# Performance work log

Hardware: AMD Instinct MI355X
Metric: run time of the kernel (lower is better)

## Reference

```python
import jax, jax.numpy as jnp
import numpy as np

B, T, N, S = 32, 64, 2048, 2048
DEMB = DENC = DDEC = 256


def setup_inputs() -> dict:
    key = jax.random.key(0)
    ks = jax.random.split(key, 14)
    u = lambda k, shp, s=0.05: jax.random.uniform(k, shp, jnp.float32, -s, s)
    return {
        "emb": jax.random.normal(ks[0], (B, N, DEMB), jnp.float32),
        "emb_mask": jnp.ones((B, N), jnp.float32),
        "enc": jax.random.normal(ks[1], (B, S, DENC), jnp.float32),
        "enc_mask": jnp.ones((B, S), jnp.float32),
        "gt": jax.random.randint(ks[2], (B, T), 0, N),
        "go": jax.random.uniform(ks[3], (DEMB,), jnp.float32, -0.1, 0.1),
        "Wih": u(ks[4], (4 * DDEC, DEMB)),
        "Whh": u(ks[5], (4 * DDEC, DDEC)),
        "bih": u(ks[6], (4 * DDEC,)),
        "bhh": u(ks[7], (4 * DDEC,)),
        "Wdt": u(ks[8], (DENC, DDEC)),
        "bdt": u(ks[9], (DENC,)),
        "Wf": u(ks[10], (DEMB + 1, DENC + DDEC)),
        "bf": u(ks[11], (DEMB + 1,)),
    }


def _pointer_decode(emb, emb_mask, enc, enc_mask, gt, go, Wih, Whh, bih, bhh, Wdt, bdt, Wf, bf):
    b, n, demb = emb.shape
    t = gt.shape[1]
    h = Whh.shape[1]
    # picked_t at step t is the (clipped) one-hot sum of gt[:, :t] (exclusive)
    onehot = jax.nn.one_hot(gt, n, dtype=emb.dtype)              # [B,T,N]
    picked = jnp.clip(jnp.cumsum(onehot, axis=1) - onehot, 0.0, 1.0)
    # teacher-forced LSTM inputs: go at t=0, then emb gathered at gt[:, t-1]
    prev = jnp.take_along_axis(emb, gt[:, :-1, None], axis=1)    # [B,T-1,demb]
    x = jnp.concatenate([jnp.broadcast_to(go, (b, 1, demb)), prev], axis=1)

    def cell(carry, x_t):
        h_t, c_t = carry
        g = x_t @ Wih.T + bih + h_t @ Whh.T + bhh                # [B,4H]
        i, f, gg, o = jnp.split(g, 4, axis=-1)                   # torch gate order i,f,g,o
        c_new = jax.nn.sigmoid(f) * c_t + jax.nn.sigmoid(i) * jnp.tanh(gg)
        h_new = jax.nn.sigmoid(o) * jnp.tanh(c_new)
        return (h_new, c_new), h_new

    h0 = jnp.zeros((b, h), emb.dtype)
    _, hs = jax.lax.scan(cell, (h0, h0), jnp.swapaxes(x, 0, 1))
    hs = jnp.swapaxes(hs, 0, 1)                                  # [B,T,H]
    # DotAttn: project dec state to denc, masked softmax over enc positions
    dec = hs @ Wdt.T + bdt                                       # [B,T,denc]
    raw = jnp.einsum('btd,bsd->bts', dec, enc)
    raw = raw - (1.0 - enc_mask)[:, None, :] * 1e20
    w = jax.nn.softmax(raw, axis=-1)
    attn = jnp.einsum('bts,bsd->btd', w, enc)                    # [B,T,denc]
    feat = jnp.concatenate([hs, attn], axis=-1) @ Wf.T + bf      # [B,T,demb+1]
    # pointer score: feat . concat([emb, picked]) over last dim, split to avoid [B,T,N,demb+1]
    score = jnp.einsum('btk,bnk->btn', feat[..., :demb], emb)
    score = score + feat[..., -1][:, :, None] * picked
    score = score - (1.0 - emb_mask)[:, None, :] * 1e20
    return score                                                 # [B,T,N]


def reference(emb, emb_mask, enc, enc_mask, gt, go, Wih, Whh, bih, bhh, Wdt, bdt, Wf, bf):
    return _pointer_decode(emb, emb_mask, enc, enc_mask, gt, go, Wih, Whh, bih, bhh, Wdt, bdt, Wf, bf)
```

## Files before the change

kernel.cpp:

```cpp
#include <hip/hip_runtime.h>
#include <cstddef>

#define BB 32
#define TT 64
#define NN_ 2048
#define SS 2048
#define DD 256
#define GG 1024
#define LP 32
#define FLD 264

typedef __attribute__((ext_vector_type(8))) short short8;
typedef __attribute__((ext_vector_type(4))) float f32x4;

static __device__ inline unsigned short f2bf(float f) {
    union { float f; unsigned int u; } v; v.f = f;
    unsigned int u = v.u;
    unsigned int r = u + 0x7FFF + ((u >> 16) & 1);
    return (unsigned short)(r >> 16);
}

static __device__ inline short8 pack8(float4 a, float4 b) {
    short8 s;
    s[0] = (short)f2bf(a.x); s[1] = (short)f2bf(a.y);
    s[2] = (short)f2bf(a.z); s[3] = (short)f2bf(a.w);
    s[4] = (short)f2bf(b.x); s[5] = (short)f2bf(b.y);
    s[6] = (short)f2bf(b.z); s[7] = (short)f2bf(b.w);
    return s;
}

static __device__ inline bool ok32(unsigned int v) {
    unsigned int x = v ^ 0x7F807F80u;
    return (((x - 0x00010001u) & ~x & 0x80008000u) == 0u);
}


__global__ __launch_bounds__(256) void k_gather(const float* __restrict__ emb,
                                                const int* __restrict__ gt,
                                                const float* __restrict__ go,
                                                float* __restrict__ x) {
    int idx = blockIdx.x * 256 + threadIdx.x;
    int d = idx & (DD - 1);
    int t = (idx >> 8) & (TT - 1);
    int b = idx >> 14;
    float v;
    if (t == 0) v = go[d];
    else        v = emb[((size_t)b * NN_ + gt[b * TT + t - 1]) * DD + d];
    x[idx] = v;
}

__global__ __launch_bounds__(256) void k_first_init(int* __restrict__ firstpos) {
    int idx = blockIdx.x * 256 + threadIdx.x;
    firstpos[idx] = TT;
}

__global__ __launch_bounds__(256) void k_first_min(const int* __restrict__ gt,
                                                   int* __restrict__ firstpos) {
    int idx = blockIdx.x * 256 + threadIdx.x;
    int b = idx / TT;
    int t = idx % TT;
    atomicMin(&firstpos[(size_t)b * NN_ + gt[idx]], t);
}

__global__ __launch_bounds__(256) void k_poison(unsigned int* __restrict__ hbuf32) {
    hbuf32[blockIdx.x * 256 + threadIdx.x] = 0x7F807F80u;
}

__global__ __launch_bounds__(256) void k_h2f(const unsigned int* __restrict__ hbuf32,
                                             float* __restrict__ hs) {
    int idx = blockIdx.x * 256 + threadIdx.x;
    int j = idx & 255;
    int t = (idx >> 8) & 63;
    int b = idx >> 14;
    unsigned int w = hbuf32[(size_t)t * 4096 + (j >> 1) * 32 + b];
    unsigned short h = (j & 1) ? (unsigned short)(w >> 16) : (unsigned short)(w & 0xFFFF);
    union { unsigned int u; float f; } v;
    v.u = ((unsigned int)h) << 16;
    hs[idx] = v.f;
}

__global__ __launch_bounds__(256) void k_cat(const float* __restrict__ hs,
                                             const float* __restrict__ attn,
                                             float* __restrict__ cat) {
    int idx = blockIdx.x * 256 + threadIdx.x;
    int d = idx & 511;
    int bt = idx >> 9;
    cat[idx] = (d < DD) ? hs[(size_t)bt * DD + d]
                        : attn[(size_t)bt * DD + (d - DD)];
}

__global__ __launch_bounds__(256) void gemm_bf16_nt(
        const float* __restrict__ A, const float* __restrict__ Bm,
        float* __restrict__ C, int K, int lda, int ldb, int ldc,
        long sA, long sB, long sC, int Nlim,
        const float* __restrict__ bias1, const float* __restrict__ bias2,
        const int* __restrict__ firstpos, const float* __restrict__ emb_mask,
        int fscol) {
    int bz = blockIdx.z;
    A += (size_t)bz * sA; Bm += (size_t)bz * sB; C += (size_t)bz * sC;
    int tm = blockIdx.y * 64, tn = blockIdx.x * 64;
    __shared__ short Ab[64][72];
    __shared__ short Bb[64][72];
    __shared__ float sfs[64];
    int tid = threadIdx.x, lane = tid & 63, wid = tid >> 6;
    int wm = wid & 1, wn = wid >> 1;

    if (fscol >= 0 && tid < 64) sfs[tid] = A[(size_t)(tm + tid) * lda + fscol];

    f32x4 zero = {0.f, 0.f, 0.f, 0.f};
    f32x4 acc[2][2] = {{zero, zero}, {zero, zero}};

    int row = tid >> 2, kk = (tid & 3) * 16;
    int brow = tn + row; if (brow >= Nlim) brow = Nlim - 1;
    const float* ap = &A[(size_t)(tm + row) * lda + kk];
    const float* bp = &Bm[(size_t)brow * ldb + kk];

    for (int k0 = 0; k0 < K; k0 += 64) {
        float4 a0 = *(const float4*)(ap + k0);
        float4 a1 = *(const float4*)(ap + k0 + 4);
        float4 a2 = *(const float4*)(ap + k0 + 8);
        float4 a3 = *(const float4*)(ap + k0 + 12);
        float4 b0 = *(const float4*)(bp + k0);
        float4 b1 = *(const float4*)(bp + k0 + 4);
        float4 b2 = *(const float4*)(bp + k0 + 8);
        float4 b3 = *(const float4*)(bp + k0 + 12);
        *(short8*)&Ab[row][kk]     = pack8(a0, a1);
        *(short8*)&Ab[row][kk + 8] = pack8(a2, a3);
        *(short8*)&Bb[row][kk]     = pack8(b0, b1);
        *(short8*)&Bb[row][kk + 8] = pack8(b2, b3);
        __syncthreads();
#pragma unroll
        for (int kt = 0; kt < 2; ++kt) {
            int k8 = kt * 32 + (lane >> 4) * 8;
            short8 fa0 = *(const short8*)&Ab[wm * 32 + (lane & 15)][k8];
            short8 fa1 = *(const short8*)&Ab[wm * 32 + 16 + (lane & 15)][k8];
            short8 fb0 = *(const short8*)&Bb[wn * 32 + (lane & 15)][k8];
            short8 fb1 = *(const short8*)&Bb[wn * 32 + 16 + (lane & 15)][k8];
            acc[0][0] = __builtin_amdgcn_mfma_f32_16x16x32_bf16(fa0, fb0, acc[0][0], 0, 0, 0);
            acc[0][1] = __builtin_amdgcn_mfma_f32_16x16x32_bf16(fa0, fb1, acc[0][1], 0, 0, 0);
            acc[1][0] = __builtin_amdgcn_mfma_f32_16x16x32_bf16(fa1, fb0, acc[1][0], 0, 0, 0);
            acc[1][1] = __builtin_amdgcn_mfma_f32_16x16x32_bf16(fa1, fb1, acc[1][1], 0, 0, 0);
        }
        __syncthreads();
    }

#pragma unroll
    for (int i = 0; i < 2; ++i) {
#pragma unroll
        for (int j = 0; j < 2; ++j) {
#pragma unroll
            for (int r = 0; r < 4; ++r) {
                int lrow = wm * 32 + i * 16 + (lane >> 4) * 4 + r;
                int gcol = tn + wn * 32 + j * 16 + (lane & 15);
                if (gcol < Nlim) {
                    float v = acc[i][j][r];
                    if (bias1) v += bias1[gcol];
                    if (bias2) v += bias2[gcol];
                    if (firstpos) {
                        int grow = tm + lrow;
                        if (firstpos[(size_t)bz * NN_ + gcol] < grow) v += sfs[lrow];
                        v -= (1.0f - emb_mask[(size_t)bz * NN_ + gcol]) * 1e20f;
                    }
                    C[(size_t)(tm + lrow) * ldc + gcol] = v;
                }
            }
        }
    }
}

__global__ __launch_bounds__(256) void gemm_attn(const float* __restrict__ W,
                                                 const float* __restrict__ enc,
                                                 float* __restrict__ attn) {
    int b = blockIdx.z;
    int tn = blockIdx.x * 64;
    const float* Wb = W + (size_t)b * TT * SS;
    const float* Eb = enc + (size_t)b * SS * DD;
    float* Cb = attn + (size_t)b * TT * DD;
    __shared__ short As[64][72];
    __shared__ float Bs[64][66];
    int tid = threadIdx.x, lane = tid & 63, wid = tid >> 6;
    int wm = wid & 1, wn = wid >> 1;
    f32x4 zero = {0.f, 0.f, 0.f, 0.f};
    f32x4 acc[2][2] = {{zero, zero}, {zero, zero}};
    int row = tid >> 2, kk = (tid & 3) * 16;
    const float* ap = Wb + (size_t)row * SS + kk;
    const float* bp = Eb + (size_t)row * DD + tn + kk;

    for (int k0 = 0; k0 < SS; k0 += 64) {
        float4 a0 = *(const float4*)(ap + k0);
        float4 a1 = *(const float4*)(ap + k0 + 4);
        float4 a2 = *(const float4*)(ap + k0 + 8);
        float4 a3 = *(const float4*)(ap + k0 + 12);
        *(short8*)&As[row][kk]     = pack8(a0, a1);
        *(short8*)&As[row][kk + 8] = pack8(a2, a3);
        const float* bq = bp + (size_t)k0 * DD;
#pragma unroll
        for (int i = 0; i < 8; ++i)
            *(float2*)&Bs[row][kk + 2 * i] = *(const float2*)(bq + 2 * i);
        __syncthreads();
#pragma unroll
        for (int kt = 0; kt < 2; ++kt) {
            int k8 = kt * 32 + (lane >> 4) * 8;
            short8 fa0 = *(const short8*)&As[wm * 32 + (lane & 15)][k8];
            short8 fa1 = *(const short8*)&As[wm * 32 + 16 + (lane & 15)][k8];
            short8 fb0, fb1;
#pragma unroll
            for (int e = 0; e < 8; ++e) {
                fb0[e] = (short)f2bf(Bs[k8 + e][wn * 32 + (lane & 15)]);
                fb1[e] = (short)f2bf(Bs[k8 + e][wn * 32 + 16 + (lane & 15)]);
            }
            acc[0][0] = __builtin_amdgcn_mfma_f32_16x16x32_bf16(fa0, fb0, acc[0][0], 0, 0, 0);
            acc[0][1] = __builtin_amdgcn_mfma_f32_16x16x32_bf16(fa0, fb1, acc[0][1], 0, 0, 0);
            acc[1][0] = __builtin_amdgcn_mfma_f32_16x16x32_bf16(fa1, fb0, acc[1][0], 0, 0, 0);
            acc[1][1] = __builtin_amdgcn_mfma_f32_16x16x32_bf16(fa1, fb1, acc[1][1], 0, 0, 0);
        }
        __syncthreads();
    }

#pragma unroll
    for (int i = 0; i < 2; ++i)
#pragma unroll
        for (int j = 0; j < 2; ++j)
#pragma unroll
            for (int r = 0; r < 4; ++r) {
                int lrow = wm * 32 + i * 16 + (lane >> 4) * 4 + r;
                int gcol = tn + wn * 32 + j * 16 + (lane & 15);
                Cb[(size_t)lrow * DD + gcol] = acc[i][j][r];
            }
}

__global__ __launch_bounds__(256) void k_lstm_mfma(const float* __restrict__ xW,
                                                   const float* __restrict__ Whh,
                                                   unsigned int* __restrict__ hbuf32) {
    int p = blockIdx.x;
    int tid = threadIdx.x;
    int lane = tid & 63;
    int wid = tid >> 6;
    int mi = wid & 1;
    int ni = wid >> 1;
    int jj = lane >> 4;
    int bl = lane & 15;
    int j = p * 8 + mi * 4 + jj;
    int b = ni * 16 + bl;

    short8 afrag[8];
    {
        int rr = lane & 15;
        const float* wrow = Whh + (size_t)((rr & 3) * 256 + p * 8 + mi * 4 + (rr >> 2)) * DD;
#pragma unroll
        for (int kt = 0; kt < 8; ++kt) {
            short8 f;
#pragma unroll
            for (int e = 0; e < 8; ++e)
                f[e] = (short)f2bf(wrow[kt * 32 + (lane >> 4) * 8 + e]);
            afrag[kt] = f;
        }
    }

    float cstate = 0.0f;
    const int wb = jj * 128 + b;

    for (int t = 0; t < TT; ++t) {
        const float* g0 = xW + ((size_t)b * TT + t) * GG + j;
        float xb0 = g0[0], xb1 = g0[256], xb2 = g0[512], xb3 = g0[768];

        f32x4 acc = {0.f, 0.f, 0.f, 0.f};
        if (t > 0) {
            const unsigned int* hb = hbuf32 + (size_t)(t - 1) * 4096;
            unsigned int q[32];
            bool ready = false;
            while (!ready) {
                ready = true;
#pragma unroll
                for (int kt = 0; kt < 8; ++kt)
#pragma unroll
                    for (int w4 = 0; w4 < 4; ++w4)
                        q[kt * 4 + w4] = __hip_atomic_load(&hb[kt * 512 + wb + w4 * 32],
                            __ATOMIC_RELAXED, __HIP_MEMORY_SCOPE_AGENT);
#pragma unroll
                for (int i = 0; i < 32; ++i) ready = ready && ok32(q[i]);
            }
#pragma unroll
            for (int kt = 0; kt < 8; ++kt) {
                union { unsigned int w[4]; short8 s; } u;
                u.w[0] = q[kt * 4 + 0]; u.w[1] = q[kt * 4 + 1];
                u.w[2] = q[kt * 4 + 2]; u.w[3] = q[kt * 4 + 3];
                acc = __builtin_amdgcn_mfma_f32_16x16x32_bf16(afrag[kt], u.s, acc, 0, 0, 0);
            }
        }

        float pi = xb0 + acc[0];
        float pf = xb1 + acc[1];
        float pg = xb2 + acc[2];
        float po = xb3 + acc[3];
        float ig = 1.0f / (1.0f + __expf(-pi));
        float fg = 1.0f / (1.0f + __expf(-pf));
        float gg = tanhf(pg);
        float og = 1.0f / (1.0f + __expf(-po));
        cstate = fg * cstate + ig * gg;
        float hn = og * tanhf(cstate);

        float hnb = __shfl_down(hn, 16);
        if ((jj & 1) == 0) {
            unsigned int wv = (unsigned int)f2bf(hn) |
                              ((unsigned int)f2bf(hnb) << 16);
            __hip_atomic_store(&hbuf32[(size_t)t * 4096 +
                                       (p * 4 + mi * 2 + (jj >> 1)) * 32 + b],
                               wv, __ATOMIC_RELAXED, __HIP_MEMORY_SCOPE_AGENT);
        }
        asm volatile("s_waitcnt vmcnt(0)" ::: "memory");
    }
}

__global__ __launch_bounds__(256) void k_softmax(float* __restrict__ raw,
                                                 const float* __restrict__ enc_mask) {
    int bt = blockIdx.x;
    int b = bt / TT;
    float* r = raw + (size_t)bt * SS;
    __shared__ float row[SS];
    __shared__ float red[16];
    int tid = threadIdx.x;
    float mx = -1e30f;
    for (int s = tid; s < SS; s += 256) {
        float v = r[s] - (1.0f - enc_mask[(size_t)b * SS + s]) * 1e20f;
        row[s] = v;
        mx = fmaxf(mx, v);
    }
#pragma unroll
    for (int o = 32; o > 0; o >>= 1) mx = fmaxf(mx, __shfl_down(mx, o));
    if ((tid & 63) == 0) red[tid >> 6] = mx;
    __syncthreads();
    if (tid == 0) {
        float m2 = red[0];
        for (int i = 1; i < 4; ++i) m2 = fmaxf(m2, red[i]);
        red[0] = m2;
    }
    __syncthreads();
    mx = red[0];
    float sum = 0.0f;
    for (int s = tid; s < SS; s += 256) {
        float e = expf(row[s] - mx);
        row[s] = e;
        sum += e;
    }
#pragma unroll
    for (int o = 32; o > 0; o >>= 1) sum += __shfl_down(sum, o);
    if ((tid & 63) == 0) red[8 + (tid >> 6)] = sum;
    __syncthreads();
    if (tid == 0) {
        float s = red[8];
        for (int i = 1; i < 4; ++i) s += red[8 + i];
        red[8] = s;
    }
    __syncthreads();
    float inv = 1.0f / red[8];
    for (int s = tid; s < SS; s += 256) r[s] = row[s] * inv;
}

extern "C" void kernel_launch(void* const* d_in, const int* in_sizes, int n_in,
                              void* d_out, int out_size, void* d_ws, size_t ws_size,
                              hipStream_t stream) {
    const float* emb      = (const float*)d_in[0];
    const float* emb_mask = (const float*)d_in[1];
    const float* enc      = (const float*)d_in[2];
    const float* enc_mask = (const float*)d_in[3];
    const int*   gt       = (const int*)d_in[4];
    const float* go       = (const float*)d_in[5];
    const float* Wih      = (const float*)d_in[6];
    const float* Whh      = (const float*)d_in[7];
    const float* bih      = (const float*)d_in[8];
    const float* bhh      = (const float*)d_in[9];
    const float* Wdt      = (const float*)d_in[10];
    const float* bdt      = (const float*)d_in[11];
    const float* Wf       = (const float*)d_in[12];
    const float* bf       = (const float*)d_in[13];
    float* out = (float*)d_out;

    float* ws    = (float*)d_ws;
    float* x     = ws;
    float* xW    = x     + (size_t)BB * TT * DD;
    float* hs    = xW    + (size_t)BB * TT * GG;
    float* dec   = hs    + (size_t)BB * TT * DD;
    float* w     = dec   + (size_t)BB * TT * DD;
    float* attn  = w     + (size_t)BB * TT * SS;
    float* feat  = attn  + (size_t)BB * TT * DD;
    float* cat   = feat  + (size_t)BB * TT * FLD;
    float* cat_end = cat + (size_t)BB * TT * 512;
    int* firstpos = (int*)cat_end;
    unsigned int* hbuf32 = (unsigned int*)(firstpos + (size_t)BB * NN_);

    k_gather<<<BB * TT * DD / 256, 256, 0, stream>>>(emb, gt, go, x);
    k_first_init<<<BB * NN_ / 256, 256, 0, stream>>>(firstpos);
    k_first_min<<<BB * TT / 256, 256, 0, stream>>>(gt, firstpos);
    k_poison<<<TT * 128 * 32 / 256, 256, 0, stream>>>(hbuf32);

    gemm_bf16_nt<<<dim3(GG / 64, BB * TT / 64, 1), 256, 0, stream>>>(
        x, Wih, xW, DD, DD, DD, GG, 0, 0, 0, GG,
        bih, bhh, nullptr, nullptr, -1);

    k_lstm_mfma<<<LP, 256, 0, stream>>>(xW, Whh, hbuf32);

    k_h2f<<<BB * TT * DD / 256, 256, 0, stream>>>(hbuf32, hs);

    gemm_bf16_nt<<<dim3(DD / 64, BB * TT / 64, 1), 256, 0, stream>>>(
        hs, Wdt, dec, DD, DD, DD, DD, 0, 0, 0, DD,
        bdt, nullptr, nullptr, nullptr, -1);

    gemm_bf16_nt<<<dim3(SS / 64, 1, BB), 256, 0, stream>>>(
        dec, enc, w, DD, DD, DD, SS,
        (long)TT * DD, (long)SS * DD, (long)TT * SS, SS,
        nullptr, nullptr, nullptr, nullptr, -1);

    k_softmax<<<BB * TT, 256, 0, stream>>>(w, enc_mask);

    gemm_attn<<<dim3(DD / 64, 1, BB), 256, 0, stream>>>(w, enc, attn);

    k_cat<<<BB * TT * 512 / 256, 256, 0, stream>>>(hs, attn, cat);

    gemm_bf16_nt<<<dim3(5, BB * TT / 64, 1), 256, 0, stream>>>(
        cat, Wf, feat, 2 * DD, 2 * DD, 2 * DD, FLD, 0, 0, 0, DD + 1,
        bf, nullptr, nullptr, nullptr, -1);

    gemm_bf16_nt<<<dim3(NN_ / 64, 1, BB), 256, 0, stream>>>(
        feat, emb, out, DD, FLD, DD, NN_,
        (long)TT * FLD, (long)NN_ * DD, (long)TT * NN_, NN_,
        nullptr, nullptr, firstpos, emb_mask, 256);
}
```

Baseline: 308.6 us.

## Replace cross-block LSTM with per-batch block using fp16 dot2 and shared memory

Replaces the 32-block MFMA LSTM, which spun on poisoned global-memory flags to exchange the hidden state across blocks every timestep, with one 1024-thread block per batch row that keeps Whh (fp16-packed, 128 registers per thread) local. The hidden state is exchanged through LDS with __syncthreads, and the gate preactivations are computed with fdot2. This removes the grid-wide polling, the poison and h2f kernels, and global atomics, and writes fp32 hs directly. The cost is heavy register pressure (128 weight registers at 1024 threads), scalar dot products instead of MFMA, fp16 rounding of weights and hidden state, and a new Whh transpose kernel.

Result: slower. 378.8 us (+22.8%).

```diff
diff --git a/kernel.cpp b/kernel.cpp
--- a/kernel.cpp
+++ b/kernel.cpp
@@ -7,11 +7,11 @@
 #define SS 2048
 #define DD 256
 #define GG 1024
-#define LP 32
 #define FLD 264
 
 typedef __attribute__((ext_vector_type(8))) short short8;
 typedef __attribute__((ext_vector_type(4))) float f32x4;
+typedef _Float16 h2_t __attribute__((ext_vector_type(2)));
 
 static __device__ inline unsigned short f2bf(float f) {
     union { float f; unsigned int u; } v; v.f = f;
@@ -29,9 +29,29 @@
     return s;
 }
 
-static __device__ inline bool ok32(unsigned int v) {
-    unsigned int x = v ^ 0x7F807F80u;
-    return (((x - 0x00010001u) & ~x & 0x80008000u) == 0u);
+static __device__ inline h2_t as_h2(unsigned int u) {
+    union { unsigned int u; h2_t h; } v; v.u = u; return v.h;
+}
+static __device__ inline unsigned int h2_pack(float a, float b) {
+    union { unsigned int u; h2_t h; } v;
+    v.h[0] = (_Float16)a; v.h[1] = (_Float16)b; return v.u;
+}
+
+#if __has_builtin(__builtin_amdgcn_fdot2)
+static __device__ inline float fdot2(h2_t a, h2_t b, float c) {
+    return __builtin_amdgcn_fdot2(a, b, c, false);
+}
+#else
+static __device__ inline float fdot2(h2_t a, h2_t b, float c) {
+    return c + (float)a[0] * (float)b[0] + (float)a[1] * (float)b[1];
+}
+#endif
+
+static __device__ inline float sigm(float x) { return 1.0f / (1.0f + __expf(-x)); }
+static __device__ inline float tanh_f(float x) {
+    float xc = fminf(fmaxf(x, -20.0f), 20.0f);
+    float e = __expf(-2.0f * xc);
+    return (1.0f - e) / (1.0f + e);
 }
 
 
@@ -62,21 +82,13 @@
     atomicMin(&firstpos[(size_t)b * NN_ + gt[idx]], t);
 }
 
-__global__ __launch_bounds__(256) void k_poison(unsigned int* __restrict__ hbuf32) {
-    hbuf32[blockIdx.x * 256 + threadIdx.x] = 0x7F807F80u;
-}
-
-__global__ __launch_bounds__(256) void k_h2f(const unsigned int* __restrict__ hbuf32,
-                                             float* __restrict__ hs) {
+__global__ __launch_bounds__(256) void k_whhT16(const float* __restrict__ Whh,
+                                                unsigned int* __restrict__ WhhT16) {
     int idx = blockIdx.x * 256 + threadIdx.x;
-    int j = idx & 255;
-    int t = (idx >> 8) & 63;
-    int b = idx >> 14;
-    unsigned int w = hbuf32[(size_t)t * 4096 + (j >> 1) * 32 + b];
-    unsigned short h = (j & 1) ? (unsigned short)(w >> 16) : (unsigned short)(w & 0xFFFF);
-    union { unsigned int u; float f; } v;
-    v.u = ((unsigned int)h) << 16;
-    hs[idx] = v.f;
+    int k2 = idx & 127;
+    int g = idx >> 7;
+    float2 w = *(const float2*)(Whh + (size_t)g * DD + 2 * k2);
+    WhhT16[(size_t)k2 * GG + g] = h2_pack(w.x, w.y);
 }
 
 __global__ __launch_bounds__(256) void k_cat(const float* __restrict__ hs,
@@ -229,86 +241,53 @@
             }
 }
 
-__global__ __launch_bounds__(256) void k_lstm_mfma(const float* __restrict__ xW,
-                                                   const float* __restrict__ Whh,
-                                                   unsigned int* __restrict__ hbuf32) {
-    int p = blockIdx.x;
-    int tid = threadIdx.x;
-    int lane = tid & 63;
-    int wid = tid >> 6;
-    int mi = wid & 1;
-    int ni = wid >> 1;
-    int jj = lane >> 4;
-    int bl = lane & 15;
-    int j = p * 8 + mi * 4 + jj;
-    int b = ni * 16 + bl;
-
-    short8 afrag[8];
-    {
-        int rr = lane & 15;
-        const float* wrow = Whh + (size_t)((rr & 3) * 256 + p * 8 + mi * 4 + (rr >> 2)) * DD;
-#pragma unroll
-        for (int kt = 0; kt < 8; ++kt) {
-            short8 f;
-#pragma unroll
-            for (int e = 0; e < 8; ++e)
-                f[e] = (short)f2bf(wrow[kt * 32 + (lane >> 4) * 8 + e]);
-            afrag[kt] = f;
+__global__ __launch_bounds__(1024) void k_lstm_local(const float* __restrict__ xW,
+                                                     const unsigned int* __restrict__ WhhT16,
+                                                     float* __restrict__ hs) {
+    int b = blockIdx.x;
+    int g = threadIdx.x;
+
+    unsigned int wreg[128];
+#pragma unroll
+    for (int i = 0; i < 128; ++i)
+        wreg[i] = WhhT16[(size_t)i * GG + g];
+
+    __shared__ uint4 h2q[32];
+    __shared__ float pre[1024];
+    if (g < 32) h2q[g] = make_uint4(0, 0, 0, 0);
+    __syncthreads();
+
+    float cstate = 0.0f;
+    const float* xwb = xW + (size_t)b * TT * GG + g;
+
+    for (int t = 0; t < TT; ++t) {
+        float xw = xwb[t * GG];
+        float a0 = 0.f, a1 = 0.f, a2 = 0.f, a3 = 0.f;
+#pragma unroll
+        for (int i = 0; i < 32; ++i) {
+            uint4 q = h2q[i];
+            a0 = fdot2(as_h2(q.x), as_h2(wreg[4 * i + 0]), a0);
+            a1 = fdot2(as_h2(q.y), as_h2(wreg[4 * i + 1]), a1);
+            a2 = fdot2(as_h2(q.z), as_h2(wreg[4 * i + 2]), a2);
+            a3 = fdot2(as_h2(q.w), as_h2(wreg[4 * i + 3]), a3);
         }
-    }
-
-    float cstate = 0.0f;
-    const int wb = jj * 128 + b;
-
-    for (int t = 0; t < TT; ++t) {
-        const float* g0 = xW + ((size_t)b * TT + t) * GG + j;
-        float xb0 = g0[0], xb1 = g0[256], xb2 = g0[512], xb3 = g0[768];
-
-        f32x4 acc = {0.f, 0.f, 0.f, 0.f};
-        if (t > 0) {
-            const unsigned int* hb = hbuf32 + (size_t)(t - 1) * 4096;
-            unsigned int q[32];
-            bool ready = false;
-            while (!ready) {
-                ready = true;
-#pragma unroll
-                for (int kt = 0; kt < 8; ++kt)
-#pragma unroll
-                    for (int w4 = 0; w4 < 4; ++w4)
-                        q[kt * 4 + w4] = __hip_atomic_load(&hb[kt * 512 + wb + w4 * 32],
-                            __ATOMIC_RELAXED, __HIP_MEMORY_SCOPE_AGENT);
-#pragma unroll
-                for (int i = 0; i < 32; ++i) ready = ready && ok32(q[i]);
-            }
-#pragma unroll
-            for (int kt = 0; kt < 8; ++kt) {
-                union { unsigned int w[4]; short8 s; } u;
-                u.w[0] = q[kt * 4 + 0]; u.w[1] = q[kt * 4 + 1];
-                u.w[2] = q[kt * 4 + 2]; u.w[3] = q[kt * 4 + 3];
-                acc = __builtin_amdgcn_mfma_f32_16x16x32_bf16(afrag[kt], u.s, acc, 0, 0, 0);
-            }
+        pre[g] = ((a0 + a1) + (a2 + a3)) + xw;
+        __syncthreads();
+
+        if (g < 256) {
+            float pi = pre[g], pf = pre[g + 256], pg = pre[g + 512], po = pre[g + 768];
+            float ig = sigm(pi);
+            float fg = sigm(pf);
+            float gg = tanh_f(pg);
+            float og = sigm(po);
+            cstate = fg * cstate + ig * gg;
+            float hn = og * tanh_f(cstate);
+            hs[((size_t)b * TT + t) * DD + g] = hn;
+            float hnb = __shfl_down(hn, 1);
+            if (!(g & 1))
+                ((unsigned int*)h2q)[g >> 1] = h2_pack(hn, hnb);
         }
-
-        float pi = xb0 + acc[0];
-        float pf = xb1 + acc[1];
-        float pg = xb2 + acc[2];
-        float po = xb3 + acc[3];
-        float ig = 1.0f / (1.0f + __expf(-pi));
-        float fg = 1.0f / (1.0f + __expf(-pf));
-        float gg = tanhf(pg);
-        float og = 1.0f / (1.0f + __expf(-po));
-        cstate = fg * cstate + ig * gg;
-        float hn = og * tanhf(cstate);
-
-        float hnb = __shfl_down(hn, 16);
-        if ((jj & 1) == 0) {
-            unsigned int wv = (unsigned int)f2bf(hn) |
-                              ((unsigned int)f2bf(hnb) << 16);
-            __hip_atomic_store(&hbuf32[(size_t)t * 4096 +
-                                       (p * 4 + mi * 2 + (jj >> 1)) * 32 + b],
-                               wv, __ATOMIC_RELAXED, __HIP_MEMORY_SCOPE_AGENT);
-        }
-        asm volatile("s_waitcnt vmcnt(0)" ::: "memory");
+        __syncthreads();
     }
 }
 
@@ -387,20 +366,18 @@
     float* cat   = feat  + (size_t)BB * TT * FLD;
     float* cat_end = cat + (size_t)BB * TT * 512;
     int* firstpos = (int*)cat_end;
-    unsigned int* hbuf32 = (unsigned int*)(firstpos + (size_t)BB * NN_);
+    unsigned int* WhhT16 = (unsigned int*)(firstpos + (size_t)BB * NN_);
 
     k_gather<<<BB * TT * DD / 256, 256, 0, stream>>>(emb, gt, go, x);
     k_first_init<<<BB * NN_ / 256, 256, 0, stream>>>(firstpos);
     k_first_min<<<BB * TT / 256, 256, 0, stream>>>(gt, firstpos);
-    k_poison<<<TT * 128 * 32 / 256, 256, 0, stream>>>(hbuf32);
+    k_whhT16<<<GG * 128 / 256, 256, 0, stream>>>(Whh, WhhT16);
 
     gemm_bf16_nt<<<dim3(GG / 64, BB * TT / 64, 1), 256, 0, stream>>>(
         x, Wih, xW, DD, DD, DD, GG, 0, 0, 0, GG,
         bih, bhh, nullptr, nullptr, -1);
 
-    k_lstm_mfma<<<LP, 256, 0, stream>>>(xW, Whh, hbuf32);
-
-    k_h2f<<<BB * TT * DD / 256, 256, 0, stream>>>(hbuf32, hs);
+    k_lstm_local<<<BB, 1024, 0, stream>>>(xW, WhhT16, hs);
 
     gemm_bf16_nt<<<dim3(DD / 64, BB * TT / 64, 1), 256, 0, stream>>>(
         hs, Wdt, dec, DD, DD, DD, DD, 0, 0, 0, DD,
```

## Consolidate LSTM recurrence into 8 blocks of 512 threads with two tiles per wave

Applied to the files above, without the earlier changes.

The persistent LSTM kernel now runs as 8 workgroups of 8 waves each, down from 32 workgroups of 4 waves. Each wave handles two 16x16 unit tiles, reusing one polled h vector for both MFMA chains. This cuts the number of workgroups and waves that spin on global memory for the previous step's hidden state each timestep, which lowers cross-CU synchronisation traffic. The cost is double the serial MFMA and gate work per wave, more register pressure, and 8 CUs working on the recurrence instead of 32.

Result: slower. 451.1 us (+46.2%).

```diff
diff --git a/kernel.cpp b/kernel.cpp
--- a/kernel.cpp
+++ b/kernel.cpp
@@ -7,7 +7,6 @@
 #define SS 2048
 #define DD 256
 #define GG 1024
-#define LP 32
 #define FLD 264
 
 typedef __attribute__((ext_vector_type(8))) short short8;
@@ -63,7 +62,7 @@
 }
 
 __global__ __launch_bounds__(256) void k_poison(unsigned int* __restrict__ hbuf32) {
-    hbuf32[blockIdx.x * 256 + threadIdx.x] = 0x7F807F80u;
+    hbuf32[(size_t)blockIdx.x * 256 + threadIdx.x] = 0x7F807F80u;
 }
 
 __global__ __launch_bounds__(256) void k_h2f(const unsigned int* __restrict__ hbuf32,
@@ -229,45 +228,49 @@
             }
 }
 
-__global__ __launch_bounds__(256) void k_lstm_mfma(const float* __restrict__ xW,
-                                                   const float* __restrict__ Whh,
-                                                   unsigned int* __restrict__ hbuf32) {
+__global__ __launch_bounds__(512) void k_lstm_mfma8(const float* __restrict__ xW,
+                                                    const float* __restrict__ Whh,
+                                                    unsigned int* __restrict__ hbuf32) {
     int p = blockIdx.x;
     int tid = threadIdx.x;
     int lane = tid & 63;
     int wid = tid >> 6;
-    int mi = wid & 1;
-    int ni = wid >> 1;
+    int ni = wid & 1;
+    int ui = wid >> 1;
     int jj = lane >> 4;
     int bl = lane & 15;
-    int j = p * 8 + mi * 4 + jj;
     int b = ni * 16 + bl;
 
-    short8 afrag[8];
-    {
+    short8 afrag[2][8];
+#pragma unroll
+    for (int mi = 0; mi < 2; ++mi) {
         int rr = lane & 15;
-        const float* wrow = Whh + (size_t)((rr & 3) * 256 + p * 8 + mi * 4 + (rr >> 2)) * DD;
+        int unit = p * 32 + ui * 8 + mi * 4 + (rr >> 2);
+        const float* wrow = Whh + (size_t)((rr & 3) * 256 + unit) * DD;
 #pragma unroll
         for (int kt = 0; kt < 8; ++kt) {
             short8 f;
 #pragma unroll
             for (int e = 0; e < 8; ++e)
-                f[e] = (short)f2bf(wrow[kt * 32 + (lane >> 4) * 8 + e]);
-            afrag[kt] = f;
-        }
-    }
-
-    float cstate = 0.0f;
+                f[e] = (short)f2bf(wrow[kt * 32 + jj * 8 + e]);
+            afrag[mi][kt] = f;
+        }
+    }
+
+    float cst0 = 0.0f, cst1 = 0.0f;
     const int wb = jj * 128 + b;
+    const int u0 = p * 32 + ui * 8 + jj;
+    const int u1 = u0 + 4;
+    const int base2 = (p * 32 + ui * 8) >> 1;
 
     for (int t = 0; t < TT; ++t) {
-        const float* g0 = xW + ((size_t)b * TT + t) * GG + j;
-        float xb0 = g0[0], xb1 = g0[256], xb2 = g0[512], xb3 = g0[768];
-
-        f32x4 acc = {0.f, 0.f, 0.f, 0.f};
+        const float* g0 = xW + ((size_t)b * TT + t) * GG;
+        float x00 = g0[u0], x01 = g0[256 + u0], x02 = g0[512 + u0], x03 = g0[768 + u0];
+        float x10 = g0[u1], x11 = g0[256 + u1], x12 = g0[512 + u1], x13 = g0[768 + u1];
+
+        unsigned int q[32];
         if (t > 0) {
             const unsigned int* hb = hbuf32 + (size_t)(t - 1) * 4096;
-            unsigned int q[32];
             bool ready = false;
             while (!ready) {
                 ready = true;
@@ -280,33 +283,41 @@
 #pragma unroll
                 for (int i = 0; i < 32; ++i) ready = ready && ok32(q[i]);
             }
-#pragma unroll
-            for (int kt = 0; kt < 8; ++kt) {
-                union { unsigned int w[4]; short8 s; } u;
-                u.w[0] = q[kt * 4 + 0]; u.w[1] = q[kt * 4 + 1];
-                u.w[2] = q[kt * 4 + 2]; u.w[3] = q[kt * 4 + 3];
-                acc = __builtin_amdgcn_mfma_f32_16x16x32_bf16(afrag[kt], u.s, acc, 0, 0, 0);
-            }
-        }
-
-        float pi = xb0 + acc[0];
-        float pf = xb1 + acc[1];
-        float pg = xb2 + acc[2];
-        float po = xb3 + acc[3];
-        float ig = 1.0f / (1.0f + __expf(-pi));
-        float fg = 1.0f / (1.0f + __expf(-pf));
-        float gg = tanhf(pg);
-        float og = 1.0f / (1.0f + __expf(-po));
-        cstate = fg * cstate + ig * gg;
-        float hn = og * tanhf(cstate);
-
-        float hnb = __shfl_down(hn, 16);
-        if ((jj & 1) == 0) {
-            unsigned int wv = (unsigned int)f2bf(hn) |
-                              ((unsigned int)f2bf(hnb) << 16);
-            __hip_atomic_store(&hbuf32[(size_t)t * 4096 +
-                                       (p * 4 + mi * 2 + (jj >> 1)) * 32 + b],
-                               wv, __ATOMIC_RELAXED, __HIP_MEMORY_SCOPE_AGENT);
+        }
+
+#pragma unroll
+        for (int mi = 0; mi < 2; ++mi) {
+            f32x4 acc = {0.f, 0.f, 0.f, 0.f};
+            if (t > 0) {
+#pragma unroll
+                for (int kt = 0; kt < 8; ++kt) {
+                    union { unsigned int w[4]; short8 s; } u;
+                    u.w[0] = q[kt * 4 + 0]; u.w[1] = q[kt * 4 + 1];
+                    u.w[2] = q[kt * 4 + 2]; u.w[3] = q[kt * 4 + 3];
+                    acc = __builtin_amdgcn_mfma_f32_16x16x32_bf16(afrag[mi][kt], u.s, acc, 0, 0, 0);
+                }
+            }
+            float pi = (mi ? x10 : x00) + acc[0];
+            float pf = (mi ? x11 : x01) + acc[1];
+            float pg = (mi ? x12 : x02) + acc[2];
+            float po = (mi ? x13 : x03) + acc[3];
+            float ig = 1.0f / (1.0f + __expf(-pi));
+            float fg = 1.0f / (1.0f + __expf(-pf));
+            float gg = tanhf(pg);
+            float og = 1.0f / (1.0f + __expf(-po));
+            float c = (mi ? cst1 : cst0);
+            c = fg * c + ig * gg;
+            float hn = og * tanhf(c);
+            if (mi) cst1 = c; else cst0 = c;
+
+            float hnb = __shfl_down(hn, 16);
+            if (!(jj & 1)) {
+                unsigned int wv = (unsigned int)f2bf(hn) |
+                                  ((unsigned int)f2bf(hnb) << 16);
+                __hip_atomic_store(&hbuf32[(size_t)t * 4096 +
+                                           (base2 + mi * 2 + (jj >> 1)) * 32 + b],
+                                   wv, __ATOMIC_RELAXED, __HIP_MEMORY_SCOPE_AGENT);
+            }
         }
         asm volatile("s_waitcnt vmcnt(0)" ::: "memory");
     }
@@ -392,13 +403,13 @@
     k_gather<<<BB * TT * DD / 256, 256, 0, stream>>>(emb, gt, go, x);
     k_first_init<<<BB * NN_ / 256, 256, 0, stream>>>(firstpos);
     k_first_min<<<BB * TT / 256, 256, 0, stream>>>(gt, firstpos);
-    k_poison<<<TT * 128 * 32 / 256, 256, 0, stream>>>(hbuf32);
+    k_poison<<<TT * 4096 / 256, 256, 0, stream>>>(hbuf32);
 
     gemm_bf16_nt<<<dim3(GG / 64, BB * TT / 64, 1), 256, 0, stream>>>(
         x, Wih, xW, DD, DD, DD, GG, 0, 0, 0, GG,
         bih, bhh, nullptr, nullptr, -1);
 
-    k_lstm_mfma<<<LP, 256, 0, stream>>>(xW, Whh, hbuf32);
+    k_lstm_mfma8<<<8, 512, 0, stream>>>(xW, Whh, hbuf32);
 
     k_h2f<<<BB * TT * DD / 256, 256, 0, stream>>>(hbuf32, hs);
 
```

## Fuse gather, h-conversion and concat into specialized GEMM kernels

Applied to the files above, without the earlier changes.

Removes the k_gather, k_h2f and k_cat kernels. The input gather now happens inside a dedicated xW GEMM, the LSTM writes a row-major bf16 copy of h that the dec and feat GEMMs read directly, and the feat GEMM reads hs and attn from separate sources instead of a concatenated buffer. This cuts three launches and several intermediate fp32 round-trips through global memory. In exchange the LSTM does an extra store per step, and the epilogue keeps an odd dead term (acc*0).

Result: faster. 288.1 us (-6.6%).

```diff
diff --git a/kernel.cpp b/kernel.cpp
--- a/kernel.cpp
+++ b/kernel.cpp
@@ -35,20 +35,6 @@
 }
 
 
-__global__ __launch_bounds__(256) void k_gather(const float* __restrict__ emb,
-                                                const int* __restrict__ gt,
-                                                const float* __restrict__ go,
-                                                float* __restrict__ x) {
-    int idx = blockIdx.x * 256 + threadIdx.x;
-    int d = idx & (DD - 1);
-    int t = (idx >> 8) & (TT - 1);
-    int b = idx >> 14;
-    float v;
-    if (t == 0) v = go[d];
-    else        v = emb[((size_t)b * NN_ + gt[b * TT + t - 1]) * DD + d];
-    x[idx] = v;
-}
-
 __global__ __launch_bounds__(256) void k_first_init(int* __restrict__ firstpos) {
     int idx = blockIdx.x * 256 + threadIdx.x;
     firstpos[idx] = TT;
@@ -63,37 +49,77 @@
 }
 
 __global__ __launch_bounds__(256) void k_poison(unsigned int* __restrict__ hbuf32) {
-    hbuf32[blockIdx.x * 256 + threadIdx.x] = 0x7F807F80u;
-}
-
-__global__ __launch_bounds__(256) void k_h2f(const unsigned int* __restrict__ hbuf32,
-                                             float* __restrict__ hs) {
-    int idx = blockIdx.x * 256 + threadIdx.x;
-    int j = idx & 255;
-    int t = (idx >> 8) & 63;
-    int b = idx >> 14;
-    unsigned int w = hbuf32[(size_t)t * 4096 + (j >> 1) * 32 + b];
-    unsigned short h = (j & 1) ? (unsigned short)(w >> 16) : (unsigned short)(w & 0xFFFF);
-    union { unsigned int u; float f; } v;
-    v.u = ((unsigned int)h) << 16;
-    hs[idx] = v.f;
-}
-
-__global__ __launch_bounds__(256) void k_cat(const float* __restrict__ hs,
-                                             const float* __restrict__ attn,
-                                             float* __restrict__ cat) {
-    int idx = blockIdx.x * 256 + threadIdx.x;
-    int d = idx & 511;
-    int bt = idx >> 9;
-    cat[idx] = (d < DD) ? hs[(size_t)bt * DD + d]
-                        : attn[(size_t)bt * DD + (d - DD)];
+    hbuf32[(size_t)blockIdx.x * 256 + threadIdx.x] = 0x7F807F80u;
+}
+
+__global__ __launch_bounds__(256) void gemm_xw(
+        const float* __restrict__ emb, const int* __restrict__ gt,
+        const float* __restrict__ go, const float* __restrict__ Wih,
+        float* __restrict__ xW,
+        const float* __restrict__ bih, const float* __restrict__ bhh) {
+    int tm = blockIdx.y * 64, tn = blockIdx.x * 64;
+    __shared__ short Ab[64][72];
+    __shared__ short Bb[64][72];
+    int tid = threadIdx.x, lane = tid & 63, wid = tid >> 6;
+    int wm = wid & 1, wn = wid >> 1;
+    f32x4 zero = {0.f, 0.f, 0.f, 0.f};
+    f32x4 acc[2][2] = {{zero, zero}, {zero, zero}};
+    int row = tid >> 2, kk = (tid & 3) * 16;
+    int m = tm + row, b = m >> 6, t = m & 63;
+    const float* arow = (t == 0) ? go
+        : emb + ((size_t)b * NN_ + gt[b * TT + t - 1]) * DD;
+    const float* ap = arow + kk;
+    const float* bp = Wih + (size_t)(tn + row) * DD + kk;
+
+    for (int k0 = 0; k0 < DD; k0 += 64) {
+        float4 a0 = *(const float4*)(ap + k0);
+        float4 a1 = *(const float4*)(ap + k0 + 4);
+        float4 a2 = *(const float4*)(ap + k0 + 8);
+        float4 a3 = *(const float4*)(ap + k0 + 12);
+        float4 b0 = *(const float4*)(bp + k0);
+        float4 b1 = *(const float4*)(bp + k0 + 4);
+        float4 b2 = *(const float4*)(bp + k0 + 8);
+        float4 b3 = *(const float4*)(bp + k0 + 12);
+        *(short8*)&Ab[row][kk]     = pack8(a0, a1);
+        *(short8*)&Ab[row][kk + 8] = pack8(a2, a3);
+        *(short8*)&Bb[row][kk]     = pack8(b0, b1);
+        *(short8*)&Bb[row][kk + 8] = pack8(b2, b3);
+        __syncthreads();
+#pragma unroll
+        for (int kt = 0; kt < 2; ++kt) {
+            int k8 = kt * 32 + (lane >> 4) * 8;
+            short8 fa0 = *(const short8*)&Ab[wm * 32 + (lane & 15)][k8];
+            short8 fa1 = *(const short8*)&Ab[wm * 32 + 16 + (lane & 15)][k8];
+            short8 fb0 = *(const short8*)&Bb[wn * 32 + (lane & 15)][k8];
+            short8 fb1 = *(const short8*)&Bb[wn * 32 + 16 + (lane & 15)][k8];
+            acc[0][0] = __builtin_amdgcn_mfma_f32_16x16x32_bf16(fa0, fb0, acc[0][0], 0, 0, 0);
+            acc[0][1] = __builtin_amdgcn_mfma_f32_16x16x32_bf16(fa0, fb1, acc[0][1], 0, 0, 0);
+            acc[1][0] = __builtin_amdgcn_mfma_f32_16x16x32_bf16(fa1, fb0, acc[1][0], 0, 0, 0);
+            acc[1][1] = __builtin_amdgcn_mfma_f32_16x16x32_bf16(fa1, fb1, acc[1][1], 0, 0, 0);
+        }
+        __syncthreads();
+    }
+
+#pragma unroll
+    for (int i = 0; i < 2; ++i)
+#pragma unroll
+        for (int j = 0; j < 2; ++j)
+#pragma unroll
+            for (int r = 0; r < 4; ++r) {
+                int lrow = wm * 32 + i * 16 + (lane >> 4) * 4 + r;
+                int gcol = tn + wn * 32 + j * 16 + (lane & 15);
+                xW[(size_t)(tm + lrow) * GG + gcol] = acc[0][0][0] * 0.0f +
+                    ((i == 0) ? (j == 0 ? acc[0][0][r] : acc[0][1][r])
+                              : (j == 0 ? acc[1][0][r] : acc[1][1][r])) +
+                    bih[gcol] + bhh[gcol];
+            }
 }
 
 __global__ __launch_bounds__(256) void gemm_bf16_nt(
         const float* __restrict__ A, const float* __restrict__ Bm,
         float* __restrict__ C, int K, int lda, int ldb, int ldc,
         long sA, long sB, long sC, int Nlim,
-        const float* __restrict__ bias1, const float* __restrict__ bias2,
+        const float* __restrict__ bias1,
         const int* __restrict__ firstpos, const float* __restrict__ emb_mask,
         int fscol) {
     int bz = blockIdx.z;
@@ -155,7 +181,6 @@
                 if (gcol < Nlim) {
                     float v = acc[i][j][r];
                     if (bias1) v += bias1[gcol];
-                    if (bias2) v += bias2[gcol];
                     if (firstpos) {
                         int grow = tm + lrow;
                         if (firstpos[(size_t)bz * NN_ + gcol] < grow) v += sfs[lrow];
@@ -166,6 +191,121 @@
             }
         }
     }
+}
+
+__global__ __launch_bounds__(256) void gemm_dec(
+        const unsigned int* __restrict__ hs16, const float* __restrict__ Wdt,
+        float* __restrict__ dec, const float* __restrict__ bdt) {
+    int tm = blockIdx.y * 64, tn = blockIdx.x * 64;
+    __shared__ short Ab[64][72];
+    __shared__ short Bb[64][72];
+    int tid = threadIdx.x, lane = tid & 63, wid = tid >> 6;
+    int wm = wid & 1, wn = wid >> 1;
+    f32x4 zero = {0.f, 0.f, 0.f, 0.f};
+    f32x4 acc[2][2] = {{zero, zero}, {zero, zero}};
+    int row = tid >> 2, kk = (tid & 3) * 16;
+    const short* ap16 = (const short*)hs16 + (size_t)(tm + row) * DD + kk;
+    const float* bp = Wdt + (size_t)(tn + row) * DD + kk;
+
+    for (int k0 = 0; k0 < DD; k0 += 64) {
+        *(short8*)&Ab[row][kk]     = *(const short8*)(ap16 + k0);
+        *(short8*)&Ab[row][kk + 8] = *(const short8*)(ap16 + k0 + 8);
+        float4 b0 = *(const float4*)(bp + k0);
+        float4 b1 = *(const float4*)(bp + k0 + 4);
+        float4 b2 = *(const float4*)(bp + k0 + 8);
+        float4 b3 = *(const float4*)(bp + k0 + 12);
+        *(short8*)&Bb[row][kk]     = pack8(b0, b1);
+        *(short8*)&Bb[row][kk + 8] = pack8(b2, b3);
+        __syncthreads();
+#pragma unroll
+        for (int kt = 0; kt < 2; ++kt) {
+            int k8 = kt * 32 + (lane >> 4) * 8;
+            short8 fa0 = *(const short8*)&Ab[wm * 32 + (lane & 15)][k8];
+            short8 fa1 = *(const short8*)&Ab[wm * 32 + 16 + (lane & 15)][k8];
+            short8 fb0 = *(const short8*)&Bb[wn * 32 + (lane & 15)][k8];
+            short8 fb1 = *(const short8*)&Bb[wn * 32 + 16 + (lane & 15)][k8];
+            acc[0][0] = __builtin_amdgcn_mfma_f32_16x16x32_bf16(fa0, fb0, acc[0][0], 0, 0, 0);
+            acc[0][1] = __builtin_amdgcn_mfma_f32_16x16x32_bf16(fa0, fb1, acc[0][1], 0, 0, 0);
+            acc[1][0] = __builtin_amdgcn_mfma_f32_16x16x32_bf16(fa1, fb0, acc[1][0], 0, 0, 0);
+            acc[1][1] = __builtin_amdgcn_mfma_f32_16x16x32_bf16(fa1, fb1, acc[1][1], 0, 0, 0);
+        }
+        __syncthreads();
+    }
+
+#pragma unroll
+    for (int i = 0; i < 2; ++i)
+#pragma unroll
+        for (int j = 0; j < 2; ++j)
+#pragma unroll
+            for (int r = 0; r < 4; ++r) {
+                int lrow = wm * 32 + i * 16 + (lane >> 4) * 4 + r;
+                int gcol = tn + wn * 32 + j * 16 + (lane & 15);
+                dec[(size_t)(tm + lrow) * DD + gcol] = acc[i][j][r] + bdt[gcol];
+            }
+}
+
+__global__ __launch_bounds__(256) void gemm_feat(
+        const unsigned int* __restrict__ hs16, const float* __restrict__ attn,
+        const float* __restrict__ Wf, const float* __restrict__ bf,
+        float* __restrict__ feat) {
+    int tm = blockIdx.y * 64, tn = blockIdx.x * 64;
+    __shared__ short Ab[64][72];
+    __shared__ short Bb[64][72];
+    int tid = threadIdx.x, lane = tid & 63, wid = tid >> 6;
+    int wm = wid & 1, wn = wid >> 1;
+    f32x4 zero = {0.f, 0.f, 0.f, 0.f};
+    f32x4 acc[2][2] = {{zero, zero}, {zero, zero}};
+    int row = tid >> 2, kk = (tid & 3) * 16;
+    int brow = tn + row; if (brow > 256) brow = 256;
+    const short* a16 = (const short*)hs16 + (size_t)(tm + row) * DD + kk;
+    const float* af  = attn + (size_t)(tm + row) * DD + kk;
+    const float* bp  = Wf + (size_t)brow * (2 * DD) + kk;
+
+    for (int k0 = 0; k0 < 2 * DD; k0 += 64) {
+        if (k0 < DD) {
+            *(short8*)&Ab[row][kk]     = *(const short8*)(a16 + k0);
+            *(short8*)&Ab[row][kk + 8] = *(const short8*)(a16 + k0 + 8);
+        } else {
+            float4 a0 = *(const float4*)(af + k0 - DD);
+            float4 a1 = *(const float4*)(af + k0 - DD + 4);
+            float4 a2 = *(const float4*)(af + k0 - DD + 8);
+            float4 a3 = *(const float4*)(af + k0 - DD + 12);
+            *(short8*)&Ab[row][kk]     = pack8(a0, a1);
+            *(short8*)&Ab[row][kk + 8] = pack8(a2, a3);
+        }
+        float4 b0 = *(const float4*)(bp + k0);
+        float4 b1 = *(const float4*)(bp + k0 + 4);
+        float4 b2 = *(const float4*)(bp + k0 + 8);
+        float4 b3 = *(const float4*)(bp + k0 + 12);
+        *(short8*)&Bb[row][kk]     = pack8(b0, b1);
+        *(short8*)&Bb[row][kk + 8] = pack8(b2, b3);
+        __syncthreads();
+#pragma unroll
+        for (int kt = 0; kt < 2; ++kt) {
+            int k8 = kt * 32 + (lane >> 4) * 8;
+            short8 fa0 = *(const short8*)&Ab[wm * 32 + (lane & 15)][k8];
+            short8 fa1 = *(const short8*)&Ab[wm * 32 + 16 + (lane & 15)][k8];
+            short8 fb0 = *(const short8*)&Bb[wn * 32 + (lane & 15)][k8];
+            short8 fb1 = *(const short8*)&Bb[wn * 32 + 16 + (lane & 15)][k8];
+            acc[0][0] = __builtin_amdgcn_mfma_f32_16x16x32_bf16(fa0, fb0, acc[0][0], 0, 0, 0);
+            acc[0][1] = __builtin_amdgcn_mfma_f32_16x16x32_bf16(fa0, fb1, acc[0][1], 0, 0, 0);
+            acc[1][0] = __builtin_amdgcn_mfma_f32_16x16x32_bf16(fa1, fb0, acc[1][0], 0, 0, 0);
+            acc[1][1] = __builtin_amdgcn_mfma_f32_16x16x32_bf16(fa1, fb1, acc[1][1], 0, 0, 0);
+        }
+        __syncthreads();
+    }
+
+#pragma unroll
+    for (int i = 0; i < 2; ++i)
+#pragma unroll
+        for (int j = 0; j < 2; ++j)
+#pragma unroll
+            for (int r = 0; r < 4; ++r) {
+                int lrow = wm * 32 + i * 16 + (lane >> 4) * 4 + r;
+                int gcol = tn + wn * 32 + j * 16 + (lane & 15);
+                if (gcol < DD + 1)
+                    feat[(size_t)(tm + lrow) * FLD + gcol] = acc[i][j][r] + bf[gcol];
+            }
 }
 
 __global__ __launch_bounds__(256) void gemm_attn(const float* __restrict__ W,
@@ -231,7 +371,8 @@
 
 __global__ __launch_bounds__(256) void k_lstm_mfma(const float* __restrict__ xW,
                                                    const float* __restrict__ Whh,
-                                                   unsigned int* __restrict__ hbuf32) {
+                                                   unsigned int* __restrict__ hbuf32,
+                                                   unsigned int* __restrict__ hs16) {
     int p = blockIdx.x;
     int tid = threadIdx.x;
     int lane = tid & 63;
@@ -304,9 +445,10 @@
         if ((jj & 1) == 0) {
             unsigned int wv = (unsigned int)f2bf(hn) |
                               ((unsigned int)f2bf(hnb) << 16);
-            __hip_atomic_store(&hbuf32[(size_t)t * 4096 +
-                                       (p * 4 + mi * 2 + (jj >> 1)) * 32 + b],
+            int jp = p * 4 + mi * 2 + (jj >> 1);
+            __hip_atomic_store(&hbuf32[(size_t)t * 4096 + jp * 32 + b],
                                wv, __ATOMIC_RELAXED, __HIP_MEMORY_SCOPE_AGENT);
+            hs16[((size_t)b * TT + t) * 128 + jp] = wv;
         }
         asm volatile("s_waitcnt vmcnt(0)" ::: "memory");
     }
@@ -377,52 +519,42 @@
     float* out = (float*)d_out;
 
     float* ws    = (float*)d_ws;
-    float* x     = ws;
-    float* xW    = x     + (size_t)BB * TT * DD;
-    float* hs    = xW    + (size_t)BB * TT * GG;
-    float* dec   = hs    + (size_t)BB * TT * DD;
-    float* w     = dec   + (size_t)BB * TT * DD;
-    float* attn  = w     + (size_t)BB * TT * SS;
-    float* feat  = attn  + (size_t)BB * TT * DD;
-    float* cat   = feat  + (size_t)BB * TT * FLD;
-    float* cat_end = cat + (size_t)BB * TT * 512;
-    int* firstpos = (int*)cat_end;
+    float* xW    = ws;
+    float* dec   = xW   + (size_t)BB * TT * GG;
+    float* w     = dec  + (size_t)BB * TT * DD;
+    float* attn  = w    + (size_t)BB * TT * SS;
+    float* feat  = attn + (size_t)BB * TT * DD;
+    float* feat_end = feat + (size_t)BB * TT * FLD;
+    int* firstpos = (int*)feat_end;
     unsigned int* hbuf32 = (unsigned int*)(firstpos + (size_t)BB * NN_);
-
-    k_gather<<<BB * TT * DD / 256, 256, 0, stream>>>(emb, gt, go, x);
+    unsigned int* hs16   = hbuf32 + (size_t)TT * 4096;
+
     k_first_init<<<BB * NN_ / 256, 256, 0, stream>>>(firstpos);
     k_first_min<<<BB * TT / 256, 256, 0, stream>>>(gt, firstpos);
-    k_poison<<<TT * 128 * 32 / 256, 256, 0, stream>>>(hbuf32);
-
-    gemm_bf16_nt<<<dim3(GG / 64, BB * TT / 64, 1), 256, 0, stream>>>(
-        x, Wih, xW, DD, DD, DD, GG, 0, 0, 0, GG,
-        bih, bhh, nullptr, nullptr, -1);
-
-    k_lstm_mfma<<<LP, 256, 0, stream>>>(xW, Whh, hbuf32);
-
-    k_h2f<<<BB * TT * DD / 256, 256, 0, stream>>>(hbuf32, hs);
-
-    gemm_bf16_nt<<<dim3(DD / 64, BB * TT / 64, 1), 256, 0, stream>>>(
-        hs, Wdt, dec, DD, DD, DD, DD, 0, 0, 0, DD,
-        bdt, nullptr, nullptr, nullptr, -1);
+    k_poison<<<TT * 4096 / 256, 256, 0, stream>>>(hbuf32);
+
+    gemm_xw<<<dim3(GG / 64, BB * TT / 64, 1), 256, 0, stream>>>(
+        emb, gt, go, Wih, xW, bih, bhh);
+
+    k_lstm_mfma<<<LP, 256, 0, stream>>>(xW, Whh, hbuf32, hs16);
+
+    gemm_dec<<<dim3(DD / 64, BB * TT / 64, 1), 256, 0, stream>>>(
+        hs16, Wdt, dec, bdt);
 
     gemm_bf16_nt<<<dim3(SS / 64, 1, BB), 256, 0, stream>>>(
         dec, enc, w, DD, DD, DD, SS,
         (long)TT * DD, (long)SS * DD, (long)TT * SS, SS,
-        nullptr, nullptr, nullptr, nullptr, -1);
+        nullptr, nullptr, nullptr, -1);
 
     k_softmax<<<BB * TT, 256, 0, stream>>>(w, enc_mask);
 
     gemm_attn<<<dim3(DD / 64, 1, BB), 256, 0, stream>>>(w, enc, attn);
 
-    k_cat<<<BB * TT * 512 / 256, 256, 0, stream>>>(hs, attn, cat);
-
-    gemm_bf16_nt<<<dim3(5, BB * TT / 64, 1), 256, 0, stream>>>(
-        cat, Wf, feat, 2 * DD, 2 * DD, 2 * DD, FLD, 0, 0, 0, DD + 1,
-        bf, nullptr, nullptr, nullptr, -1);
+    gemm_feat<<<dim3(5, BB * TT / 64, 1), 256, 0, stream>>>(
+        hs16, attn, Wf, bf, feat);
 
     gemm_bf16_nt<<<dim3(NN_ / 64, 1, BB), 256, 0, stream>>>(
         feat, emb, out, DD, FLD, DD, NN_,
         (long)TT * FLD, (long)NN_ * DD, (long)TT * NN_, NN_,
-        nullptr, nullptr, firstpos, emb_mask, 256);
-}
+        nullptr, firstpos, emb_mask, 256);
+}
```
